# Optimization experiments

Hardware: AMD Instinct MI355X
Metric: run time of the kernel (lower is better)

The kernel has to match this reference:

```python
import jax, jax.numpy as jnp
import numpy as np

B, L, H, Di, N, K, R = 2, 512, 2048, 4096, 16, 4, 128


def setup_inputs() -> dict:
    key = jax.random.key(0)
    ks = jax.random.split(key, 8)
    s = 0.02
    inp = {
        "x": jax.random.normal(ks[0], (B, L, H), jnp.float32),
        "in_w": jax.random.normal(ks[1], (2 * Di, H), jnp.float32) * s,
        "in_b": jnp.zeros((2 * Di,), jnp.float32),
        "conv_w": jax.random.normal(ks[2], (Di, 1, K), jnp.float32) * s,  # depthwise conv weight
        "conv_b": jnp.zeros((Di,), jnp.float32),
        "xproj_w": jax.random.normal(ks[3], (R + 2 * N, Di), jnp.float32) * s,
        "dt_w": jax.random.normal(ks[4], (Di, R), jnp.float32) * s,
        "dt_b": jax.random.normal(ks[5], (Di,), jnp.float32) * 0.1,
        "A_log": jnp.log(jnp.broadcast_to(jnp.arange(1, N + 1, dtype=jnp.float32)[None, :], (Di, N))) + jnp.zeros((Di, N), jnp.float32),
        "D": jnp.ones((Di,), jnp.float32),
        "out_w": jax.random.normal(ks[6], (H, Di), jnp.float32) * s,
        "out_b": jnp.zeros((H,), jnp.float32),
    }
    return inp


def reference(x, in_w, in_b, conv_w, conv_b, xproj_w, dt_w, dt_b, A_log, D, out_w, out_b):
    silu = jax.nn.silu
    # in_proj -> split into hidden path and gate
    proj = x @ in_w.T + in_b                       # [B, L, 2*Di]
    h, gate = jnp.split(proj, 2, axis=-1)          # each [B, L, Di]
    # causal depthwise conv1d over time
    hc = jnp.transpose(h, (0, 2, 1))               # [B, Di, L]
    hc = jax.lax.conv_general_dilated(
        hc, conv_w, window_strides=(1,), padding=[(K - 1, 0)],
        dimension_numbers=("NCH", "OIH", "NCH"), feature_group_count=Di)
    hc = silu(hc + conv_b[None, :, None])          # [B, Di, L]
    hs = jnp.transpose(hc, (0, 2, 1))              # [B, L, Di]
    # input-dependent SSM parameters
    sp = hs @ xproj_w.T                            # [B, L, R + 2N]
    ts, Bm, Cm = sp[..., :R], sp[..., R:R + N], sp[..., R + N:]
    dt = jax.nn.softplus(ts @ dt_w.T + dt_b)       # [B, L, Di]
    A = -jnp.exp(A_log)                            # [Di, N]
    dA = jnp.exp(dt[..., None] * A[None, None])    # [B, L, Di, N]
    dBu = dt[..., None] * Bm[:, :, None, :] * hs[..., None]  # [B, L, Di, N]

    # selective scan: s_t = dA_t * s_{t-1} + dBu_t ; y_t = s_t . C_t
    def step(s, inputs):
        dA_t, dBu_t, C_t = inputs                  # [B,Di,N], [B,Di,N], [B,N]
        s = dA_t * s + dBu_t
        y = jnp.einsum("bdn,bn->bd", s, C_t)
        return s, y

    s0 = jnp.zeros((x.shape[0], Di, N), x.dtype)
    _, ys = jax.lax.scan(step, s0, (jnp.swapaxes(dA, 0, 1), jnp.swapaxes(dBu, 0, 1), jnp.swapaxes(Cm, 0, 1)))
    y = jnp.transpose(ys, (1, 0, 2))               # [B, L, Di]
    y = (y + hs * D) * silu(gate)
    return y @ out_w.T + out_b                     # [B, L, H]
```

## Files before the change

kernel.cpp:

```cpp
#include <hip/hip_runtime.h>
#include <hip/hip_bf16.h>

typedef __hip_bfloat16 bf16;
typedef short bf16x8 __attribute__((ext_vector_type(8)));
typedef float f32x4 __attribute__((ext_vector_type(4)));

#define BB 2
#define LL 512
#define HH 2048
#define DI 4096
#define NST 16
#define KK 4
#define RR 128
#define BLM (BB*LL)
#define CN 16
#define LC (LL/CN)
#define ZXP 16
#define ZOUT 4

enum { MODE_PROJ = 0, MODE_XPROJ = 1, MODE_DT = 2, MODE_OUT = 3 };

__device__ __forceinline__ float sigmoidf_(float x) { return 1.f / (1.f + __expf(-x)); }
__device__ __forceinline__ float softplusf_(float x) {
    return fmaxf(x, 0.f) + log1pf(__expf(-fabsf(x)));
}
__device__ __forceinline__ unsigned int bfpack(float a, float b) {
    __hip_bfloat162 h = __float22bfloat162_rn(make_float2(a, b));
    union { __hip_bfloat162 h; unsigned int u; } cv; cv.h = h;
    return cv.u;
}

typedef const __attribute__((address_space(1))) unsigned int* gas_t;
typedef __attribute__((address_space(3))) unsigned int* las_t;
__device__ __forceinline__ void gld16(const void* g, void* l) {
    __builtin_amdgcn_global_load_lds((gas_t)g, (las_t)l, 16, 0, 0);
}

__global__ __launch_bounds__(256) void cvt_f32_bf16(
    const float* __restrict__ src, bf16* __restrict__ dst, int n4)
{
    int i = blockIdx.x * 256 + threadIdx.x;
    int stride = gridDim.x * 256;
    for (; i < n4; i += stride) {
        float4 v = ((const float4*)src)[i];
        uint2 o; o.x = bfpack(v.x, v.y); o.y = bfpack(v.z, v.w);
        ((uint2*)dst)[i] = o;
    }
}

template<int BM, int MODE, bool AF32>
__global__ __launch_bounds__(256) void gemm_bf16(
    const void* __restrict__ Ap, const bf16* __restrict__ Bw,
    int N, int K, int lda, int ldb,
    const float* __restrict__ bias,
    float* __restrict__ outf, bf16* __restrict__ outh,
    float* __restrict__ s0, float* __restrict__ s1,
    float* __restrict__ s2, float* __restrict__ s3)
{
    __shared__ short sA[BM * 32];
    __shared__ short sB[128 * 32];
    const int tid = threadIdx.x;
    const int col0 = blockIdx.x * 128;
    const int row0 = blockIdx.y * BM;
    const int wave = tid >> 6;
    const int lane = tid & 63;
    constexpr int NJ = (BM == 128) ? 4 : 2;
    const int wr = (BM == 128) ? ((wave >> 1) * 64) : 0;
    const int wc = (BM == 128) ? ((wave & 1) * 64) : (wave * 32);
    const int lr = lane & 15;
    const int kq = (lane >> 4) << 3;

    const int kpb = K / gridDim.z;
    const int kbeg = blockIdx.z * kpb;
    const int kend = kbeg + kpb;

    const int r0 = tid >> 2;
    const int kc = (tid & 3) << 3;

    f32x4 acc[4][NJ] = {};

    for (int k0 = kbeg; k0 < kend; k0 += 32) {
        #pragma unroll
        for (int p = 0; p < BM / 64; p++) {
            int r = r0 + p * 64;
            if (AF32) {
                const float* ap = (const float*)Ap + (size_t)(row0 + r) * lda + k0 + kc;
                float4 a0 = *(const float4*)ap;
                float4 a1 = *(const float4*)(ap + 4);
                *(uint4*)(&sA[r * 32 + kc]) = make_uint4(
                    bfpack(a0.x, a0.y), bfpack(a0.z, a0.w),
                    bfpack(a1.x, a1.y), bfpack(a1.z, a1.w));
            } else {
                gld16((const bf16*)Ap + (size_t)(row0 + r) * lda + k0 + kc,
                      &sA[r * 32 + kc]);
            }
        }
        #pragma unroll
        for (int p = 0; p < 2; p++) {
            int rr = r0 + p * 64;
            int nb = col0 + rr; if (nb > N - 1) nb = N - 1;
            gld16(Bw + (size_t)nb * ldb + k0 + kc, &sB[rr * 32 + kc]);
        }
        __syncthreads();
        bf16x8 af[4], bfr[NJ];
        #pragma unroll
        for (int i = 0; i < 4; i++)
            af[i] = *(const bf16x8*)(&sA[(wr + i * 16 + lr) * 32 + kq]);
        #pragma unroll
        for (int j = 0; j < NJ; j++)
            bfr[j] = *(const bf16x8*)(&sB[(wc + j * 16 + lr) * 32 + kq]);
        #pragma unroll
        for (int i = 0; i < 4; i++)
            #pragma unroll
            for (int j = 0; j < NJ; j++)
                acc[i][j] = __builtin_amdgcn_mfma_f32_16x16x32_bf16(af[i], bfr[j], acc[i][j], 0, 0, 0);
        __syncthreads();
    }

    float* oslice = outf;
    if (MODE == MODE_OUT) {
        int z = blockIdx.z;
        oslice = (z == 0) ? s0 : (z == 1) ? s1 : (z == 2) ? s2 : s3;
    }
    const int drow = (lane >> 4) << 2;
    const int dcol = lane & 15;
    #pragma unroll
    for (int i = 0; i < 4; i++) {
        #pragma unroll
        for (int j = 0; j < NJ; j++) {
            int n = col0 + wc + j * 16 + dcol;
            if (n >= N) continue;
            float bv = bias ? bias[n] : 0.f;
            #pragma unroll
            for (int r = 0; r < 4; r++) {
                int m = row0 + wr + i * 16 + drow + r;
                float v = acc[i][j][r];
                if (MODE == MODE_PROJ) {
                    v += bv;
                    if (n < DI) outf[(size_t)m * DI + n] = v;
                    else        outh[(size_t)m * DI + (n - DI)] = (bf16)v;
                } else if (MODE == MODE_XPROJ) {
                    outf[(size_t)blockIdx.z * (BLM * 160) + (size_t)m * 160 + n] = v;
                } else if (MODE == MODE_DT) {
                    outf[(size_t)m * DI + n] = softplusf_(v + bv);
                } else {
                    oslice[(size_t)m * HH + n] = v;
                }
            }
        }
    }
}

__global__ __launch_bounds__(256) void reduce_sp(
    const float* __restrict__ spS, float* __restrict__ sp_f, bf16* __restrict__ ts_b)
{
    int i = blockIdx.x * 256 + threadIdx.x;
    int row = i / 40, c4 = (i % 40) * 4;
    float4 s = make_float4(0.f, 0.f, 0.f, 0.f);
    #pragma unroll
    for (int z = 0; z < ZXP; z++) {
        float4 v = *(const float4*)&spS[(size_t)z * (BLM * 160) + (size_t)row * 160 + c4];
        s.x += v.x; s.y += v.y; s.z += v.z; s.w += v.w;
    }
    *(float4*)&sp_f[(size_t)row * 160 + c4] = s;
    if (c4 < RR) {
        uint2 o; o.x = bfpack(s.x, s.y); o.y = bfpack(s.z, s.w);
        *(uint2*)&ts_b[(size_t)row * RR + c4] = o;
    }
}

__global__ __launch_bounds__(256) void reduce_out(
    const float* __restrict__ s0, const float* __restrict__ s1,
    const float* __restrict__ s2, const float* __restrict__ s3,
    const float* __restrict__ bias, float* __restrict__ out)
{
    int i = blockIdx.x * 256 + threadIdx.x;
    int c4 = (i & 511) << 2;
    float4 a = ((const float4*)s0)[i];
    float4 b = ((const float4*)s1)[i];
    float4 c = ((const float4*)s2)[i];
    float4 d = ((const float4*)s3)[i];
    float4 bv = *(const float4*)&bias[c4];
    float4 r;
    r.x = a.x + b.x + c.x + d.x + bv.x;
    r.y = a.y + b.y + c.y + d.y + bv.y;
    r.z = a.z + b.z + c.z + d.z + bv.z;
    r.w = a.w + b.w + c.w + d.w + bv.w;
    ((float4*)out)[i] = r;
}

__global__ __launch_bounds__(256) void conv_silu(
    const float* __restrict__ h, const float* __restrict__ conv_w,
    const float* __restrict__ conv_b, bf16* __restrict__ hs_b)
{
    int idx = blockIdx.x * 256 + threadIdx.x;
    int d = idx & (DI - 1);
    int l = (idx >> 12) & (LL - 1);
    float acc = conv_b[d];
    #pragma unroll
    for (int k = 0; k < KK; k++) {
        int ls = l - (KK - 1) + k;
        if (ls >= 0) acc += h[(size_t)idx + (size_t)(ls - l) * DI] * conv_w[d * KK + k];
    }
    float s = acc * sigmoidf_(acc);
    hs_b[idx] = (bf16)s;
}

__global__ __launch_bounds__(256) void scan_part1(
    const float* __restrict__ dtr, const float* __restrict__ sp,
    const bf16* __restrict__ hs_b, const float* __restrict__ A_log,
    float* __restrict__ P_ws, float* __restrict__ S_ws)
{
    int bid = blockIdx.x;
    int c  = bid & (CN - 1);
    int db = (bid >> 4) & (DI / 256 - 1);
    int b  = bid >> 8;
    int d  = db * 256 + threadIdx.x;

    float A[NST], P[NST], S[NST];
    #pragma unroll
    for (int n = 0; n < NST; n++) {
        A[n] = -__expf(A_log[d * NST + n]);
        P[n] = 1.f; S[n] = 0.f;
    }
    const float* spb = sp + (size_t)b * LL * 160;
    size_t base = (size_t)b * LL * DI + d;
    for (int l = c * LC; l < (c + 1) * LC; l++) {
        size_t off = base + (size_t)l * DI;
        float dtv = dtr[off];
        float hsv = (float)hs_b[off];
        float dh = dtv * hsv;
        #pragma unroll
        for (int n = 0; n < NST; n++) {
            float a  = __expf(dtv * A[n]);
            float Bn = spb[l * 160 + RR + n];
            S[n] = a * S[n] + dh * Bn;
            P[n] *= a;
        }
    }
    size_t o = ((size_t)((b * CN + c) * DI) + d) * NST;
    #pragma unroll
    for (int q = 0; q < 4; q++) {
        *(float4*)&P_ws[o + q * 4] = make_float4(P[q*4], P[q*4+1], P[q*4+2], P[q*4+3]);
        *(float4*)&S_ws[o + q * 4] = make_float4(S[q*4], S[q*4+1], S[q*4+2], S[q*4+3]);
    }
}

__global__ __launch_bounds__(256) void scan_part2(
    const float* __restrict__ dtr, const float* __restrict__ sp,
    const bf16* __restrict__ hs_b, const bf16* __restrict__ g_b,
    const float* __restrict__ A_log, const float* __restrict__ Dv,
    const float* __restrict__ P_ws, const float* __restrict__ S_ws,
    bf16* __restrict__ y_b)
{
    int bid = blockIdx.x;
    int c  = bid & (CN - 1);
    int db = (bid >> 4) & (DI / 256 - 1);
    int b  = bid >> 8;
    int d  = db * 256 + threadIdx.x;

    float s[NST];
    #pragma unroll
    for (int n = 0; n < NST; n++) s[n] = 0.f;
    for (int j = 0; j < c; j++) {
        size_t o = ((size_t)((b * CN + j) * DI) + d) * NST;
        #pragma unroll
        for (int q = 0; q < 4; q++) {
            float4 Pq = *(const float4*)&P_ws[o + q * 4];
            float4 Sq = *(const float4*)&S_ws[o + q * 4];
            s[q*4+0] = Pq.x * s[q*4+0] + Sq.x;
            s[q*4+1] = Pq.y * s[q*4+1] + Sq.y;
            s[q*4+2] = Pq.z * s[q*4+2] + Sq.z;
            s[q*4+3] = Pq.w * s[q*4+3] + Sq.w;
        }
    }

    float A[NST];
    #pragma unroll
    for (int n = 0; n < NST; n++) A[n] = -__expf(A_log[d * NST + n]);
    float Dd = Dv[d];

    const float* spb = sp + (size_t)b * LL * 160;
    size_t base = (size_t)b * LL * DI + d;
    for (int l = c * LC; l < (c + 1) * LC; l++) {
        size_t off = base + (size_t)l * DI;
        float dtv = dtr[off];
        float hsv = (float)hs_b[off];
        float dh = dtv * hsv;
        float y = 0.f;
        #pragma unroll
        for (int n = 0; n < NST; n++) {
            float a  = __expf(dtv * A[n]);
            float Bn = spb[l * 160 + RR + n];
            float Cn = spb[l * 160 + RR + NST + n];
            s[n] = a * s[n] + dh * Bn;
            y += s[n] * Cn;
        }
        float gv = (float)g_b[off];
        y_b[off] = (bf16)((y + hsv * Dd) * (gv * sigmoidf_(gv)));
    }
}

extern "C" void kernel_launch(void* const* d_in, const int* in_sizes, int n_in,
                              void* d_out, int out_size, void* d_ws, size_t ws_size,
                              hipStream_t stream)
{
    const float* x       = (const float*)d_in[0];
    const float* in_w    = (const float*)d_in[1];
    const float* in_b    = (const float*)d_in[2];
    const float* conv_w  = (const float*)d_in[3];
    const float* conv_b  = (const float*)d_in[4];
    const float* xproj_w = (const float*)d_in[5];
    const float* dt_w    = (const float*)d_in[6];
    const float* dt_b    = (const float*)d_in[7];
    const float* A_log   = (const float*)d_in[8];
    const float* Dv      = (const float*)d_in[9];
    const float* out_w   = (const float*)d_in[10];
    const float* out_b   = (const float*)d_in[11];
    float* out = (float*)d_out;

    char* ws = (char*)d_ws;
    const size_t MB = 1u << 20;
    bf16*  in_w_b = (bf16*)(ws);
    float* spS    = (float*)(ws);
    float* P_ws   = (float*)(ws);
    float* S_ws   = (float*)(ws + 8 * MB);
    bf16*  y_b    = (bf16*)(ws + 16 * MB);
    float* oS0    = (float*)(ws + 24 * MB);
    float* oS1    = (float*)(ws);
    float* h_dt   = (float*)(ws + 32 * MB);
    bf16*  ow_b   = (bf16*)(ws + 32 * MB);
    float* oS2    = (float*)(ws + 48 * MB);
    bf16*  g_b    = (bf16*)(ws + 48 * MB);
    float* oS3    = (float*)(ws + 56 * MB);
    bf16*  hs_b   = (bf16*)(ws + 56 * MB);
    char* p = ws + 64 * MB;
    float* sp_f = (float*)p; p += (size_t)BLM * 160 * 4;
    bf16*  ts_b = (bf16*)p;  p += (size_t)BLM * RR * 2;
    bf16*  xw_b = (bf16*)p;  p += (size_t)(RR + 2 * NST) * DI * 2;
    bf16*  dtw_b= (bf16*)p;  p += (size_t)DI * RR * 2;

    cvt_f32_bf16<<<512, 256, 0, stream>>>(in_w, in_w_b, 2 * DI * HH / 4);
    cvt_f32_bf16<<<640, 256, 0, stream>>>(xproj_w, xw_b, (RR + 2 * NST) * DI / 4);
    cvt_f32_bf16<<<512, 256, 0, stream>>>(dt_w, dtw_b, DI * RR / 4);
    gemm_bf16<128, MODE_PROJ, true><<<dim3((2 * DI) / 128, BLM / 128, 1), 256, 0, stream>>>(
        x, in_w_b, 2 * DI, HH, HH, HH, in_b, h_dt, g_b, nullptr, nullptr, nullptr, nullptr);
    conv_silu<<<(BLM * DI) / 256, 256, 0, stream>>>(h_dt, conv_w, conv_b, hs_b);
    gemm_bf16<64, MODE_XPROJ, false><<<dim3(2, BLM / 64, ZXP), 256, 0, stream>>>(
        hs_b, xw_b, RR + 2 * NST, DI, DI, DI, nullptr, spS, nullptr, nullptr, nullptr, nullptr, nullptr);
    reduce_sp<<<160, 256, 0, stream>>>(spS, sp_f, ts_b);
    gemm_bf16<64, MODE_DT, false><<<dim3(DI / 128, BLM / 64, 1), 256, 0, stream>>>(
        ts_b, dtw_b, DI, RR, RR, RR, dt_b, h_dt, nullptr, nullptr, nullptr, nullptr, nullptr);
    scan_part1<<<BB * (DI / 256) * CN, 256, 0, stream>>>(
        h_dt, sp_f, hs_b, A_log, P_ws, S_ws);
    scan_part2<<<BB * (DI / 256) * CN, 256, 0, stream>>>(
        h_dt, sp_f, hs_b, g_b, A_log, Dv, P_ws, S_ws, y_b);
    cvt_f32_bf16<<<512, 256, 0, stream>>>(out_w, ow_b, HH * DI / 4);
    gemm_bf16<128, MODE_OUT, false><<<dim3(HH / 128, BLM / 128, ZOUT), 256, 0, stream>>>(
        y_b, ow_b, HH, DI, DI, DI, nullptr, nullptr, nullptr, oS0, oS1, oS2, oS3);
    reduce_out<<<2048, 256, 0, stream>>>(oS0, oS1, oS2, oS3, out_b, out);
}
```

Measured before the change: 407.1 us.

## Pre-convert x to bf16, merge weight casts, store h as bf16

Converts x to bf16 in one merged conversion kernel together with the in_proj, xproj and dt weights, replacing three launches with one. The in_proj GEMM then loads A through direct global-to-LDS copies instead of converting fp32 on the fly. The hidden path h is written as bf16 instead of fp32, which halves its write and the conv read traffic. The workspace layout is reshuffled to fit the new buffers. The cost is an extra pass over x and extra bf16 rounding of h before the conv.

New measurement: 375.1 us. 7.9% less time.

```diff
diff --git a/kernel.cpp b/kernel.cpp
--- a/kernel.cpp
+++ b/kernel.cpp
@@ -36,24 +36,43 @@
     __builtin_amdgcn_global_load_lds((gas_t)g, (las_t)l, 16, 0, 0);
 }
 
+__device__ __forceinline__ void cvt_seg(const float* s, bf16* d, int i) {
+    float4 v = ((const float4*)s)[i];
+    uint2 o; o.x = bfpack(v.x, v.y); o.y = bfpack(v.z, v.w);
+    ((uint2*)d)[i] = o;
+}
+
+__global__ __launch_bounds__(256) void cvt_all(
+    const float* __restrict__ s0, bf16* __restrict__ d0, int n0,
+    const float* __restrict__ s1, bf16* __restrict__ d1, int n1,
+    const float* __restrict__ s2, bf16* __restrict__ d2, int n2,
+    const float* __restrict__ s3, bf16* __restrict__ d3, int n3)
+{
+    int i = blockIdx.x * 256 + threadIdx.x;
+    int stride = gridDim.x * 256;
+    int t1 = n0 + n1, t2 = t1 + n2, t3 = t2 + n3;
+    for (; i < t3; i += stride) {
+        if      (i < n0) cvt_seg(s0, d0, i);
+        else if (i < t1) cvt_seg(s1, d1, i - n0);
+        else if (i < t2) cvt_seg(s2, d2, i - t1);
+        else             cvt_seg(s3, d3, i - t2);
+    }
+}
+
 __global__ __launch_bounds__(256) void cvt_f32_bf16(
     const float* __restrict__ src, bf16* __restrict__ dst, int n4)
 {
     int i = blockIdx.x * 256 + threadIdx.x;
     int stride = gridDim.x * 256;
-    for (; i < n4; i += stride) {
-        float4 v = ((const float4*)src)[i];
-        uint2 o; o.x = bfpack(v.x, v.y); o.y = bfpack(v.z, v.w);
-        ((uint2*)dst)[i] = o;
-    }
-}
-
-template<int BM, int MODE, bool AF32>
+    for (; i < n4; i += stride) cvt_seg(src, dst, i);
+}
+
+template<int BM, int MODE>
 __global__ __launch_bounds__(256) void gemm_bf16(
-    const void* __restrict__ Ap, const bf16* __restrict__ Bw,
+    const bf16* __restrict__ A, const bf16* __restrict__ Bw,
     int N, int K, int lda, int ldb,
     const float* __restrict__ bias,
-    float* __restrict__ outf, bf16* __restrict__ outh,
+    float* __restrict__ outf, bf16* __restrict__ outh, bf16* __restrict__ outh2,
     float* __restrict__ s0, float* __restrict__ s1,
     float* __restrict__ s2, float* __restrict__ s3)
 {
@@ -83,17 +102,7 @@
         #pragma unroll
         for (int p = 0; p < BM / 64; p++) {
             int r = r0 + p * 64;
-            if (AF32) {
-                const float* ap = (const float*)Ap + (size_t)(row0 + r) * lda + k0 + kc;
-                float4 a0 = *(const float4*)ap;
-                float4 a1 = *(const float4*)(ap + 4);
-                *(uint4*)(&sA[r * 32 + kc]) = make_uint4(
-                    bfpack(a0.x, a0.y), bfpack(a0.z, a0.w),
-                    bfpack(a1.x, a1.y), bfpack(a1.z, a1.w));
-            } else {
-                gld16((const bf16*)Ap + (size_t)(row0 + r) * lda + k0 + kc,
-                      &sA[r * 32 + kc]);
-            }
+            gld16(A + (size_t)(row0 + r) * lda + k0 + kc, &sA[r * 32 + kc]);
         }
         #pragma unroll
         for (int p = 0; p < 2; p++) {
@@ -137,7 +146,7 @@
                 float v = acc[i][j][r];
                 if (MODE == MODE_PROJ) {
                     v += bv;
-                    if (n < DI) outf[(size_t)m * DI + n] = v;
+                    if (n < DI) outh2[(size_t)m * DI + n] = (bf16)v;
                     else        outh[(size_t)m * DI + (n - DI)] = (bf16)v;
                 } else if (MODE == MODE_XPROJ) {
                     outf[(size_t)blockIdx.z * (BLM * 160) + (size_t)m * 160 + n] = v;
@@ -190,7 +199,7 @@
 }
 
 __global__ __launch_bounds__(256) void conv_silu(
-    const float* __restrict__ h, const float* __restrict__ conv_w,
+    const bf16* __restrict__ h, const float* __restrict__ conv_w,
     const float* __restrict__ conv_b, bf16* __restrict__ hs_b)
 {
     int idx = blockIdx.x * 256 + threadIdx.x;
@@ -200,7 +209,7 @@
     #pragma unroll
     for (int k = 0; k < KK; k++) {
         int ls = l - (KK - 1) + k;
-        if (ls >= 0) acc += h[(size_t)idx + (size_t)(ls - l) * DI] * conv_w[d * KK + k];
+        if (ls >= 0) acc += (float)h[(size_t)idx + (size_t)(ls - l) * DI] * conv_w[d * KK + k];
     }
     float s = acc * sigmoidf_(acc);
     hs_b[idx] = (bf16)s;
@@ -321,42 +330,50 @@
 
     char* ws = (char*)d_ws;
     const size_t MB = 1u << 20;
-    bf16*  in_w_b = (bf16*)(ws);
+    bf16*  x_b    = (bf16*)(ws);
     float* spS    = (float*)(ws);
     float* P_ws   = (float*)(ws);
     float* S_ws   = (float*)(ws + 8 * MB);
+    float* oS1    = (float*)(ws);
+    bf16*  in_w_b = (bf16*)(ws + 16 * MB);
     bf16*  y_b    = (bf16*)(ws + 16 * MB);
+    bf16*  hs_b   = (bf16*)(ws + 24 * MB);
     float* oS0    = (float*)(ws + 24 * MB);
-    float* oS1    = (float*)(ws);
-    float* h_dt   = (float*)(ws + 32 * MB);
+    float* dt_f   = (float*)(ws + 32 * MB);
     bf16*  ow_b   = (bf16*)(ws + 32 * MB);
+    bf16*  h_b    = (bf16*)(ws + 48 * MB);
     float* oS2    = (float*)(ws + 48 * MB);
-    bf16*  g_b    = (bf16*)(ws + 48 * MB);
+    bf16*  g_b    = (bf16*)(ws + 56 * MB);
     float* oS3    = (float*)(ws + 56 * MB);
-    bf16*  hs_b   = (bf16*)(ws + 56 * MB);
     char* p = ws + 64 * MB;
     float* sp_f = (float*)p; p += (size_t)BLM * 160 * 4;
     bf16*  ts_b = (bf16*)p;  p += (size_t)BLM * RR * 2;
     bf16*  xw_b = (bf16*)p;  p += (size_t)(RR + 2 * NST) * DI * 2;
     bf16*  dtw_b= (bf16*)p;  p += (size_t)DI * RR * 2;
 
-    cvt_f32_bf16<<<512, 256, 0, stream>>>(in_w, in_w_b, 2 * DI * HH / 4);
-    cvt_f32_bf16<<<640, 256, 0, stream>>>(xproj_w, xw_b, (RR + 2 * NST) * DI / 4);
-    cvt_f32_bf16<<<512, 256, 0, stream>>>(dt_w, dtw_b, DI * RR / 4);
-    gemm_bf16<128, MODE_PROJ, true><<<dim3((2 * DI) / 128, BLM / 128, 1), 256, 0, stream>>>(
-        x, in_w_b, 2 * DI, HH, HH, HH, in_b, h_dt, g_b, nullptr, nullptr, nullptr, nullptr);
-    conv_silu<<<(BLM * DI) / 256, 256, 0, stream>>>(h_dt, conv_w, conv_b, hs_b);
-    gemm_bf16<64, MODE_XPROJ, false><<<dim3(2, BLM / 64, ZXP), 256, 0, stream>>>(
-        hs_b, xw_b, RR + 2 * NST, DI, DI, DI, nullptr, spS, nullptr, nullptr, nullptr, nullptr, nullptr);
+    cvt_all<<<2048, 256, 0, stream>>>(
+        x, x_b, BLM * HH / 4,
+        in_w, in_w_b, 2 * DI * HH / 4,
+        xproj_w, xw_b, (RR + 2 * NST) * DI / 4,
+        dt_w, dtw_b, DI * RR / 4);
+    gemm_bf16<128, MODE_PROJ><<<dim3((2 * DI) / 128, BLM / 128, 1), 256, 0, stream>>>(
+        x_b, in_w_b, 2 * DI, HH, HH, HH, in_b, nullptr, g_b, h_b,
+        nullptr, nullptr, nullptr, nullptr);
+    conv_silu<<<(BLM * DI) / 256, 256, 0, stream>>>(h_b, conv_w, conv_b, hs_b);
+    gemm_bf16<64, MODE_XPROJ><<<dim3(2, BLM / 64, ZXP), 256, 0, stream>>>(
+        hs_b, xw_b, RR + 2 * NST, DI, DI, DI, nullptr, spS, nullptr, nullptr,
+        nullptr, nullptr, nullptr, nullptr);
     reduce_sp<<<160, 256, 0, stream>>>(spS, sp_f, ts_b);
-    gemm_bf16<64, MODE_DT, false><<<dim3(DI / 128, BLM / 64, 1), 256, 0, stream>>>(
-        ts_b, dtw_b, DI, RR, RR, RR, dt_b, h_dt, nullptr, nullptr, nullptr, nullptr, nullptr);
+    gemm_bf16<64, MODE_DT><<<dim3(DI / 128, BLM / 64, 1), 256, 0, stream>>>(
+        ts_b, dtw_b, DI, RR, RR, RR, dt_b, dt_f, nullptr, nullptr,
+        nullptr, nullptr, nullptr, nullptr);
     scan_part1<<<BB * (DI / 256) * CN, 256, 0, stream>>>(
-        h_dt, sp_f, hs_b, A_log, P_ws, S_ws);
+        dt_f, sp_f, hs_b, A_log, P_ws, S_ws);
     scan_part2<<<BB * (DI / 256) * CN, 256, 0, stream>>>(
-        h_dt, sp_f, hs_b, g_b, A_log, Dv, P_ws, S_ws, y_b);
+        dt_f, sp_f, hs_b, g_b, A_log, Dv, P_ws, S_ws, y_b);
     cvt_f32_bf16<<<512, 256, 0, stream>>>(out_w, ow_b, HH * DI / 4);
-    gemm_bf16<128, MODE_OUT, false><<<dim3(HH / 128, BLM / 128, ZOUT), 256, 0, stream>>>(
-        y_b, ow_b, HH, DI, DI, DI, nullptr, nullptr, nullptr, oS0, oS1, oS2, oS3);
+    gemm_bf16<128, MODE_OUT><<<dim3(HH / 128, BLM / 128, ZOUT), 256, 0, stream>>>(
+        y_b, ow_b, HH, DI, DI, DI, nullptr, nullptr, nullptr, nullptr,
+        oS0, oS1, oS2, oS3);
     reduce_out<<<2048, 256, 0, stream>>>(oS0, oS1, oS2, oS3, out_b, out);
 }
```
